# Kernel tuning notes

Measured on AMD Instinct MI355X. Metric: run time of the kernel, lower is better.

Reference implementation:

```python
import jax, jax.numpy as jnp
import numpy as np


def setup_inputs() -> dict:
    key = jax.random.key(0)
    ks = jax.random.split(key, 10)
    B, L, H, E, D = 2, 2048, 16, 64, 64
    d_model = 512
    inp = {
        "queries": jax.random.normal(ks[0], (B, L, H, E), jnp.float32),
        "keys": jax.random.normal(ks[1], (B, L, H, E), jnp.float32),
        "values": jax.random.normal(ks[2], (B, L, H, D), jnp.float32),
        "raw_series": jax.random.normal(ks[3], (B, L, d_model), jnp.float32),
        # learned fusion MLP: Linear(d_model, d_model//2) -> ReLU -> Linear(d_model//2, 1)
        "w1": jax.random.normal(ks[4], (d_model, d_model // 2), jnp.float32) / np.sqrt(d_model),
        "b1": jnp.zeros((d_model // 2,), jnp.float32),
        "w2": jax.random.normal(ks[5], (d_model // 2, 1), jnp.float32) / np.sqrt(d_model // 2),
        "b2": jnp.zeros((1,), jnp.float32),
        # per-head trend scaling, init ones
        "alpha_trend": jnp.ones((H,), jnp.float32),
    }
    return inp


MOMENTUM_ALPHA = 1.0
MOMENTUM_K = 1


def reference(queries, keys, values, raw_series, w1, b1, w2, b2, alpha_trend):
    B, L, H, E = queries.shape
    scale = 1.0 / jnp.sqrt(jnp.asarray(E, queries.dtype))

    # ---- soft momentum bias ----
    # learned fusion: MLP over features -> scalar per position, [B, L]
    h = jax.nn.relu(raw_series @ w1 + b1)
    fused = (h @ w2 + b2)[..., 0]                       # [B, L]
    k = max(1, min(MOMENTUM_K, L - 1))
    momentum = fused[:, k:] - fused[:, :-k]              # [B, L-k]
    momentum = jnp.pad(momentum, ((0, 0), (k, 0)))       # left-pad zeros -> [B, L]
    diff = jnp.abs(momentum[:, :, None] - momentum[:, None, :])  # [B, L, L]
    soft_bias = -MOMENTUM_ALPHA * diff                   # [B, L, L]

    # ---- attention ----
    scores = jnp.einsum('blhe,bshe->bhls', queries, keys)  # [B, H, L, L]
    scores = scores + soft_bias[:, None, :, :] * alpha_trend[None, :, None, None]
    causal = jnp.triu(jnp.ones((L, L), bool), k=1)       # True above diagonal
    scores = jnp.where(causal[None, None], -jnp.inf, scores)
    A = jax.nn.softmax(scale * scores, axis=-1)          # [B, H, L, L]
    V = jnp.einsum('bhls,bshd->blhd', A, values)         # [B, L, H, D]
    return V
```

## Files before the change

kernel.cpp:

```cpp
#include <hip/hip_runtime.h>
#include <math.h>

#define B_ 2
#define L_ 2048
#define H_ 16
#define E_ 64
#define D_ 64
#define DM_ 512
#define DH_ 256

typedef __bf16 bf16_t;
typedef bf16_t bf16x8_t __attribute__((ext_vector_type(8)));
typedef float f32x4_t __attribute__((ext_vector_type(4)));

__device__ __forceinline__ unsigned bpack(float hi, float lo) {
    unsigned uh = __float_as_uint(hi) + 0x8000u;
    unsigned ul = __float_as_uint(lo) + 0x8000u;
    return __builtin_amdgcn_perm(uh, ul, 0x07060302u);
}

__device__ __forceinline__ bf16_t to_bf16(float f) {
    union { float f; unsigned u; } x; x.f = f;
    unsigned r = (x.u + 0x7fffu + ((x.u >> 16) & 1u)) >> 16;
    union { unsigned short s; bf16_t b; } y; y.s = (unsigned short)r;
    return y.b;
}

__global__ __launch_bounds__(256) void transpose_w1_kernel(
        const float* __restrict__ w1, bf16_t* __restrict__ w1t) {
    const int n = blockIdx.x;
    const int t = threadIdx.x;
    #pragma unroll
    for (int u = 0; u < 2; ++u) {
        int k = t + u * 256;
        float v = w1[(size_t)k * DH_ + n];
        w1t[(size_t)n * DM_ + k] = to_bf16(v);
    }
}

__global__ __launch_bounds__(256) void mlp_kernel(
        const float* __restrict__ raw, const bf16_t* __restrict__ w1t,
        const float* __restrict__ b1, const float* __restrict__ w2,
        const float* __restrict__ b2, float* __restrict__ fused) {
    __shared__ bf16_t Rs[16][520];
    __shared__ float part[4][16];
    const int t = threadIdx.x;
    const int m0 = blockIdx.x * 16;
    #pragma unroll
    for (int u = 0; u < 8; ++u) {
        int idx = t + u * 256;
        int row = idx >> 7;
        int k = (idx & 127) << 2;
        f32x4_t v = *(const f32x4_t*)&raw[(size_t)(m0 + row) * DM_ + k];
        uint2 p;
        p.x = bpack(v[1], v[0]);
        p.y = bpack(v[3], v[2]);
        *(uint2*)&Rs[row][k] = p;
    }
    __syncthreads();
    const int wave = t >> 6;
    const int lane = t & 63;
    const int lrow = lane & 15;
    const int lgrp = lane >> 4;
    const int n0w = wave * 64;

    f32x4_t acc[4];
    #pragma unroll
    for (int nt = 0; nt < 4; ++nt) acc[nt] = (f32x4_t){0.f, 0.f, 0.f, 0.f};

    const bf16_t* wbase = w1t + (size_t)(n0w + lrow) * DM_ + lgrp * 8;
    #pragma unroll
    for (int s = 0; s < 16; ++s) {
        bf16x8_t a = *(const bf16x8_t*)&Rs[lrow][s * 32 + lgrp * 8];
        #pragma unroll
        for (int nt = 0; nt < 4; ++nt) {
            bf16x8_t b = *(const bf16x8_t*)(wbase + nt * 16 * DM_ + s * 32);
            acc[nt] = __builtin_amdgcn_mfma_f32_16x16x32_bf16(a, b, acc[nt], 0, 0, 0);
        }
    }
    float rowpart[4] = {0.f, 0.f, 0.f, 0.f};
    #pragma unroll
    for (int nt = 0; nt < 4; ++nt) {
        int n = n0w + nt * 16 + lrow;
        float b1v = b1[n];
        float w2v = w2[n];
        #pragma unroll
        for (int r = 0; r < 4; ++r) {
            float h = acc[nt][r] + b1v;
            h = h > 0.f ? h : 0.f;
            rowpart[r] += h * w2v;
        }
    }
    #pragma unroll
    for (int r = 0; r < 4; ++r) {
        float v = rowpart[r];
        v += __shfl_xor(v, 1);
        v += __shfl_xor(v, 2);
        v += __shfl_xor(v, 4);
        v += __shfl_xor(v, 8);
        if (lrow == 0) part[wave][lgrp * 4 + r] = v;
    }
    __syncthreads();
    if (t < 16)
        fused[m0 + t] = part[0][t] + part[1][t] + part[2][t] + part[3][t] + b2[0];
}

__global__ __launch_bounds__(256) void momentum_kernel(
        const float* __restrict__ fused, float* __restrict__ mom) {
    int i = blockIdx.x * 256 + threadIdx.x;
    if (i < B_ * L_) {
        int l = i & (L_ - 1);
        mom[i] = (l == 0) ? 0.f : fused[i] - fused[i - 1];
    }
}

struct TileRegs { f32x4_t k[4]; float v[16]; float m; };

__global__ __launch_bounds__(256) void attn_kernel(
        const float* __restrict__ Q, const float* __restrict__ K,
        const float* __restrict__ V, const float* __restrict__ mom,
        const float* __restrict__ alpha_trend, float* __restrict__ out) {
    __shared__ bf16_t Ks[64][72];
    __shared__ bf16_t Vt[64][72];
    __shared__ unsigned short Ps[4][16][68];
    __shared__ float moms[64];

    const int bid  = blockIdx.x;
    const int bh   = bid & 31;
    const int qt   = 31 - (bid >> 5);
    const int h    = bh & 15;
    const int b    = bh >> 4;
    const int q0   = qt << 6;
    const int tid  = threadIdx.x;
    const int wave = tid >> 6;
    const int lane = tid & 63;
    const int lrow = lane & 15;
    const int lgrp = lane >> 4;

    const float c1     = 0.18033688f;
    const float ascale2 = alpha_trend[h] * c1;
    const size_t bl    = (size_t)b * L_;
    const int qw0      = q0 + wave * 16;

    const float* Kb   = K + ((bl)*H_ + h) * E_;
    const float* Vb   = V + ((bl)*H_ + h) * D_;
    const float* momp = mom + bl;

    const int krow = tid >> 4;
    const int ke0  = (tid & 15) << 2;
    const int vd   = tid & 63;
    const int vsb  = tid >> 6;

    bf16x8_t a_lo, a_hi;
    {
        const float* qp = Q + ((bl + qw0 + lrow) * H_ + h) * E_ + lgrp * 8;
        f32x4_t v0 = *(const f32x4_t*)(qp);
        f32x4_t v1 = *(const f32x4_t*)(qp + 4);
        f32x4_t v2 = *(const f32x4_t*)(qp + 32);
        f32x4_t v3 = *(const f32x4_t*)(qp + 36);
        #pragma unroll
        for (int k = 0; k < 4; ++k) {
            a_lo[k]     = to_bf16(v0[k] * c1);
            a_lo[4 + k] = to_bf16(v1[k] * c1);
            a_hi[k]     = to_bf16(v2[k] * c1);
            a_hi[4 + k] = to_bf16(v3[k] * c1);
        }
    }
    float mq[4];
    #pragma unroll
    for (int r = 0; r < 4; ++r) mq[r] = momp[qw0 + lgrp * 4 + r];

    f32x4_t Oacc[4];
    #pragma unroll
    for (int c = 0; c < 4; ++c) Oacc[c] = (f32x4_t){0.f, 0.f, 0.f, 0.f};
    float rowsum[4] = {0.f, 0.f, 0.f, 0.f};

    TileRegs tr;
    {
        #pragma unroll
        for (int u = 0; u < 4; ++u)
            tr.k[u] = *(const f32x4_t*)&Kb[(krow + u * 16) * (H_ * E_) + ke0];
        #pragma unroll
        for (int j = 0; j < 16; ++j)
            tr.v[j] = Vb[(vsb * 16 + j) * (H_ * D_) + vd];
        tr.m = (tid < 64) ? momp[tid] : 0.f;
    }

    for (int st = 0; st <= qt; ++st) {
        __syncthreads();
        #pragma unroll
        for (int u = 0; u < 4; ++u) {
            uint2 p;
            p.x = bpack(tr.k[u][1], tr.k[u][0]);
            p.y = bpack(tr.k[u][3], tr.k[u][2]);
            *(uint2*)&Ks[krow + u * 16][ke0] = p;
        }
        #pragma unroll
        for (int u = 0; u < 4; ++u) {
            uint2 p;
            p.x = bpack(tr.v[u * 4 + 1], tr.v[u * 4 + 0]);
            p.y = bpack(tr.v[u * 4 + 3], tr.v[u * 4 + 2]);
            *(uint2*)&Vt[vd][vsb * 16 + u * 4] = p;
        }
        if (tid < 64) moms[tid] = tr.m;
        __syncthreads();

        if (st < qt) {
            const int s0n = (st + 1) << 6;
            #pragma unroll
            for (int u = 0; u < 4; ++u)
                tr.k[u] = *(const f32x4_t*)&Kb[(s0n + krow + u * 16) * (H_ * E_) + ke0];
            #pragma unroll
            for (int j = 0; j < 16; ++j)
                tr.v[j] = Vb[(s0n + vsb * 16 + j) * (H_ * D_) + vd];
            tr.m = (tid < 64) ? momp[s0n + tid] : 0.f;
        }

        f32x4_t Sacc[4];
        #pragma unroll
        for (int c = 0; c < 4; ++c) Sacc[c] = (f32x4_t){0.f, 0.f, 0.f, 0.f};
        #pragma unroll
        for (int c = 0; c < 4; ++c) {
            bf16x8_t b_lo = *(const bf16x8_t*)&Ks[c * 16 + lrow][lgrp * 8];
            bf16x8_t b_hi = *(const bf16x8_t*)&Ks[c * 16 + lrow][32 + lgrp * 8];
            Sacc[c] = __builtin_amdgcn_mfma_f32_16x16x32_bf16(a_lo, b_lo, Sacc[c], 0, 0, 0);
            Sacc[c] = __builtin_amdgcn_mfma_f32_16x16x32_bf16(a_hi, b_hi, Sacc[c], 0, 0, 0);
        }

        float rowe[4][4];
        #pragma unroll
        for (int c = 0; c < 4; ++c) {
            float ms = moms[c * 16 + lrow];
            #pragma unroll
            for (int r = 0; r < 4; ++r) {
                float arg = Sacc[c][r] - ascale2 * fabsf(mq[r] - ms);
                rowe[c][r] = __builtin_amdgcn_exp2f(arg);
            }
        }
        if (st == qt) {
            const int s0 = st << 6;
            #pragma unroll
            for (int c = 0; c < 4; ++c) {
                int sg = s0 + c * 16 + lrow;
                #pragma unroll
                for (int r = 0; r < 4; ++r)
                    if (sg > qw0 + lgrp * 4 + r) rowe[c][r] = 0.f;
            }
        }
        unsigned short* Psw = &Ps[wave][0][0];
        #pragma unroll
        for (int c = 0; c < 4; ++c) {
            #pragma unroll
            for (int r = 0; r < 4; ++r) {
                unsigned u = (__float_as_uint(rowe[c][r]) + 0x8000u) & 0xffff0000u;
                Psw[(lgrp * 4 + r) * 68 + c * 16 + lrow] = (unsigned short)(u >> 16);
                rowsum[r] += __uint_as_float(u);
            }
        }

        #pragma unroll
        for (int hh = 0; hh < 2; ++hh) {
            union { uint2 u2[2]; bf16x8_t v; } ab;
            ab.u2[0] = *(const uint2*)&Psw[lrow * 68 + hh * 32 + lgrp * 8];
            ab.u2[1] = *(const uint2*)&Psw[lrow * 68 + hh * 32 + lgrp * 8 + 4];
            #pragma unroll
            for (int c2 = 0; c2 < 4; ++c2) {
                bf16x8_t bv = *(const bf16x8_t*)&Vt[c2 * 16 + lrow][hh * 32 + lgrp * 8];
                Oacc[c2] = __builtin_amdgcn_mfma_f32_16x16x32_bf16(ab.v, bv, Oacc[c2], 0, 0, 0);
            }
        }
    }

    #pragma unroll
    for (int r = 0; r < 4; ++r) {
        float rs = rowsum[r];
        rs += __shfl_xor(rs, 1);
        rs += __shfl_xor(rs, 2);
        rs += __shfl_xor(rs, 4);
        rs += __shfl_xor(rs, 8);
        float inv = 1.f / rs;
        size_t orow = ((bl + qw0 + lgrp * 4 + r) * H_ + h) * D_;
        #pragma unroll
        for (int c = 0; c < 4; ++c)
            out[orow + c * 16 + lrow] = Oacc[c][r] * inv;
    }
}

extern "C" void kernel_launch(void* const* d_in, const int* in_sizes, int n_in,
                              void* d_out, int out_size, void* d_ws, size_t ws_size,
                              hipStream_t stream) {
    const float* Q     = (const float*)d_in[0];
    const float* K     = (const float*)d_in[1];
    const float* V     = (const float*)d_in[2];
    const float* raw   = (const float*)d_in[3];
    const float* w1    = (const float*)d_in[4];
    const float* b1    = (const float*)d_in[5];
    const float* w2    = (const float*)d_in[6];
    const float* b2    = (const float*)d_in[7];
    const float* alpha = (const float*)d_in[8];
    float* out = (float*)d_out;

    float* fused = (float*)d_ws;
    float* mom   = fused + B_ * L_;
    bf16_t* w1t  = (bf16_t*)(mom + B_ * L_);

    transpose_w1_kernel<<<DH_, 256, 0, stream>>>(w1, w1t);
    mlp_kernel<<<B_ * L_ / 16, 256, 0, stream>>>(raw, w1t, b1, w2, b2, fused);
    momentum_kernel<<<(B_ * L_ + 255) / 256, 256, 0, stream>>>(fused, mom);
    attn_kernel<<<B_ * H_ * (L_ / 64), 256, 0, stream>>>(Q, K, V, mom, alpha, out);
}
```

Baseline: 162.8 us.

## Double-buffer attention K/V tiles, fold momentum into attention, split MLP K across waves

```diff
diff --git a/kernel.cpp b/kernel.cpp
--- a/kernel.cpp
+++ b/kernel.cpp
@@ -38,17 +38,18 @@
     }
 }
 
-__global__ __launch_bounds__(256) void mlp_kernel(
+__global__ __launch_bounds__(512) void mlp_kernel(
         const float* __restrict__ raw, const bf16_t* __restrict__ w1t,
         const float* __restrict__ b1, const float* __restrict__ w2,
         const float* __restrict__ b2, float* __restrict__ fused) {
     __shared__ bf16_t Rs[16][520];
+    __shared__ float pk[4][4][16][17];
     __shared__ float part[4][16];
     const int t = threadIdx.x;
     const int m0 = blockIdx.x * 16;
     #pragma unroll
-    for (int u = 0; u < 8; ++u) {
-        int idx = t + u * 256;
+    for (int u = 0; u < 4; ++u) {
+        int idx = t + u * 512;
         int row = idx >> 7;
         int k = (idx & 127) << 2;
         f32x4_t v = *(const f32x4_t*)&raw[(size_t)(m0 + row) * DM_ + k];
@@ -62,68 +63,72 @@
     const int lane = t & 63;
     const int lrow = lane & 15;
     const int lgrp = lane >> 4;
-    const int n0w = wave * 64;
+    const int nq   = wave & 3;
+    const int kh   = wave >> 2;
+    const int n0w  = nq * 64;
+    const int k0   = kh * 256;
 
     f32x4_t acc[4];
     #pragma unroll
     for (int nt = 0; nt < 4; ++nt) acc[nt] = (f32x4_t){0.f, 0.f, 0.f, 0.f};
 
-    const bf16_t* wbase = w1t + (size_t)(n0w + lrow) * DM_ + lgrp * 8;
-    #pragma unroll
-    for (int s = 0; s < 16; ++s) {
-        bf16x8_t a = *(const bf16x8_t*)&Rs[lrow][s * 32 + lgrp * 8];
+    const bf16_t* wbase = w1t + (size_t)(n0w + lrow) * DM_ + k0 + lgrp * 8;
+    #pragma unroll
+    for (int s = 0; s < 8; ++s) {
+        bf16x8_t a = *(const bf16x8_t*)&Rs[lrow][k0 + s * 32 + lgrp * 8];
         #pragma unroll
         for (int nt = 0; nt < 4; ++nt) {
             bf16x8_t b = *(const bf16x8_t*)(wbase + nt * 16 * DM_ + s * 32);
             acc[nt] = __builtin_amdgcn_mfma_f32_16x16x32_bf16(a, b, acc[nt], 0, 0, 0);
         }
     }
-    float rowpart[4] = {0.f, 0.f, 0.f, 0.f};
-    #pragma unroll
-    for (int nt = 0; nt < 4; ++nt) {
-        int n = n0w + nt * 16 + lrow;
-        float b1v = b1[n];
-        float w2v = w2[n];
+    if (kh == 1) {
+        #pragma unroll
+        for (int nt = 0; nt < 4; ++nt)
+            #pragma unroll
+            for (int r = 0; r < 4; ++r)
+                pk[nq][nt][lgrp * 4 + r][lrow] = acc[nt][r];
+    }
+    __syncthreads();
+    if (kh == 0) {
+        float rowpart[4] = {0.f, 0.f, 0.f, 0.f};
+        #pragma unroll
+        for (int nt = 0; nt < 4; ++nt) {
+            int n = n0w + nt * 16 + lrow;
+            float b1v = b1[n];
+            float w2v = w2[n];
+            #pragma unroll
+            for (int r = 0; r < 4; ++r) {
+                float h = acc[nt][r] + pk[nq][nt][lgrp * 4 + r][lrow] + b1v;
+                h = h > 0.f ? h : 0.f;
+                rowpart[r] += h * w2v;
+            }
+        }
         #pragma unroll
         for (int r = 0; r < 4; ++r) {
-            float h = acc[nt][r] + b1v;
-            h = h > 0.f ? h : 0.f;
-            rowpart[r] += h * w2v;
-        }
-    }
-    #pragma unroll
-    for (int r = 0; r < 4; ++r) {
-        float v = rowpart[r];
-        v += __shfl_xor(v, 1);
-        v += __shfl_xor(v, 2);
-        v += __shfl_xor(v, 4);
-        v += __shfl_xor(v, 8);
-        if (lrow == 0) part[wave][lgrp * 4 + r] = v;
+            float v = rowpart[r];
+            v += __shfl_xor(v, 1);
+            v += __shfl_xor(v, 2);
+            v += __shfl_xor(v, 4);
+            v += __shfl_xor(v, 8);
+            if (lrow == 0) part[nq][lgrp * 4 + r] = v;
+        }
     }
     __syncthreads();
     if (t < 16)
         fused[m0 + t] = part[0][t] + part[1][t] + part[2][t] + part[3][t] + b2[0];
 }
 
-__global__ __launch_bounds__(256) void momentum_kernel(
-        const float* __restrict__ fused, float* __restrict__ mom) {
-    int i = blockIdx.x * 256 + threadIdx.x;
-    if (i < B_ * L_) {
-        int l = i & (L_ - 1);
-        mom[i] = (l == 0) ? 0.f : fused[i] - fused[i - 1];
-    }
-}
-
 struct TileRegs { f32x4_t k[4]; float v[16]; float m; };
 
 __global__ __launch_bounds__(256) void attn_kernel(
         const float* __restrict__ Q, const float* __restrict__ K,
-        const float* __restrict__ V, const float* __restrict__ mom,
+        const float* __restrict__ V, const float* __restrict__ fused,
         const float* __restrict__ alpha_trend, float* __restrict__ out) {
-    __shared__ bf16_t Ks[64][72];
-    __shared__ bf16_t Vt[64][72];
+    __shared__ bf16_t Ks[2][64][72];
+    __shared__ bf16_t Vt[2][64][76];
     __shared__ unsigned short Ps[4][16][68];
-    __shared__ float moms[64];
+    __shared__ float moms[2][64];
 
     const int bid  = blockIdx.x;
     const int bh   = bid & 31;
@@ -137,14 +142,14 @@
     const int lrow = lane & 15;
     const int lgrp = lane >> 4;
 
-    const float c1     = 0.18033688f;
+    const float c1      = 0.18033688f;
     const float ascale2 = alpha_trend[h] * c1;
-    const size_t bl    = (size_t)b * L_;
-    const int qw0      = q0 + wave * 16;
-
-    const float* Kb   = K + ((bl)*H_ + h) * E_;
-    const float* Vb   = V + ((bl)*H_ + h) * D_;
-    const float* momp = mom + bl;
+    const size_t bl     = (size_t)b * L_;
+    const int qw0       = q0 + wave * 16;
+
+    const float* Kb = K + (bl * H_ + h) * E_;
+    const float* Vb = V + (bl * H_ + h) * D_;
+    const float* fp = fused + bl;
 
     const int krow = tid >> 4;
     const int ke0  = (tid & 15) << 2;
@@ -168,7 +173,10 @@
     }
     float mq[4];
     #pragma unroll
-    for (int r = 0; r < 4; ++r) mq[r] = momp[qw0 + lgrp * 4 + r];
+    for (int r = 0; r < 4; ++r) {
+        int l = qw0 + lgrp * 4 + r;
+        mq[r] = (l == 0) ? 0.f : fp[l] - fp[l - 1];
+    }
 
     f32x4_t Oacc[4];
     #pragma unroll
@@ -176,53 +184,55 @@
     float rowsum[4] = {0.f, 0.f, 0.f, 0.f};
 
     TileRegs tr;
-    {
-        #pragma unroll
-        for (int u = 0; u < 4; ++u)
-            tr.k[u] = *(const f32x4_t*)&Kb[(krow + u * 16) * (H_ * E_) + ke0];
-        #pragma unroll
-        for (int j = 0; j < 16; ++j)
-            tr.v[j] = Vb[(vsb * 16 + j) * (H_ * D_) + vd];
-        tr.m = (tid < 64) ? momp[tid] : 0.f;
-    }
+    #define LOAD_TILE(st_) do {                                                   \
+        const int s0_ = (st_) << 6;                                               \
+        _Pragma("unroll")                                                         \
+        for (int u = 0; u < 4; ++u)                                               \
+            tr.k[u] = *(const f32x4_t*)&Kb[(s0_ + krow + u * 16) * (H_ * E_) + ke0]; \
+        _Pragma("unroll")                                                         \
+        for (int j = 0; j < 16; ++j)                                              \
+            tr.v[j] = Vb[(s0_ + vsb * 16 + j) * (H_ * D_) + vd];                  \
+        if (tid < 64) {                                                           \
+            int l_ = s0_ + tid;                                                   \
+            tr.m = (l_ == 0) ? 0.f : fp[l_] - fp[l_ - 1];                         \
+        }                                                                         \
+    } while (0)
+
+    #define STAGE_TILE(pb_) do {                                                  \
+        _Pragma("unroll")                                                         \
+        for (int u = 0; u < 4; ++u) {                                             \
+            uint2 p;                                                              \
+            p.x = bpack(tr.k[u][1], tr.k[u][0]);                                  \
+            p.y = bpack(tr.k[u][3], tr.k[u][2]);                                  \
+            *(uint2*)&Ks[pb_][krow + u * 16][ke0] = p;                            \
+        }                                                                         \
+        _Pragma("unroll")                                                         \
+        for (int u = 0; u < 4; ++u) {                                             \
+            uint2 p;                                                              \
+            p.x = bpack(tr.v[u * 4 + 1], tr.v[u * 4 + 0]);                        \
+            p.y = bpack(tr.v[u * 4 + 3], tr.v[u * 4 + 2]);                        \
+            *(uint2*)&Vt[pb_][vd][vsb * 16 + u * 4] = p;                          \
+        }                                                                         \
+        if (tid < 64) moms[pb_][tid] = tr.m;                                      \
+    } while (0)
+
+    LOAD_TILE(0);
+    STAGE_TILE(0);
+    if (qt >= 1) LOAD_TILE(1);
+    __syncthreads();
 
     for (int st = 0; st <= qt; ++st) {
-        __syncthreads();
-        #pragma unroll
-        for (int u = 0; u < 4; ++u) {
-            uint2 p;
-            p.x = bpack(tr.k[u][1], tr.k[u][0]);
-            p.y = bpack(tr.k[u][3], tr.k[u][2]);
-            *(uint2*)&Ks[krow + u * 16][ke0] = p;
-        }
-        #pragma unroll
-        for (int u = 0; u < 4; ++u) {
-            uint2 p;
-            p.x = bpack(tr.v[u * 4 + 1], tr.v[u * 4 + 0]);
-            p.y = bpack(tr.v[u * 4 + 3], tr.v[u * 4 + 2]);
-            *(uint2*)&Vt[vd][vsb * 16 + u * 4] = p;
-        }
-        if (tid < 64) moms[tid] = tr.m;
-        __syncthreads();
-
-        if (st < qt) {
-            const int s0n = (st + 1) << 6;
-            #pragma unroll
-            for (int u = 0; u < 4; ++u)
-                tr.k[u] = *(const f32x4_t*)&Kb[(s0n + krow + u * 16) * (H_ * E_) + ke0];
-            #pragma unroll
-            for (int j = 0; j < 16; ++j)
-                tr.v[j] = Vb[(s0n + vsb * 16 + j) * (H_ * D_) + vd];
-            tr.m = (tid < 64) ? momp[s0n + tid] : 0.f;
-        }
+        const int cb = st & 1;
+        if (st < qt) STAGE_TILE((st + 1) & 1);
+        if (st + 2 <= qt) LOAD_TILE(st + 2);
 
         f32x4_t Sacc[4];
         #pragma unroll
         for (int c = 0; c < 4; ++c) Sacc[c] = (f32x4_t){0.f, 0.f, 0.f, 0.f};
         #pragma unroll
         for (int c = 0; c < 4; ++c) {
-            bf16x8_t b_lo = *(const bf16x8_t*)&Ks[c * 16 + lrow][lgrp * 8];
-            bf16x8_t b_hi = *(const bf16x8_t*)&Ks[c * 16 + lrow][32 + lgrp * 8];
+            bf16x8_t b_lo = *(const bf16x8_t*)&Ks[cb][c * 16 + lrow][lgrp * 8];
+            bf16x8_t b_hi = *(const bf16x8_t*)&Ks[cb][c * 16 + lrow][32 + lgrp * 8];
             Sacc[c] = __builtin_amdgcn_mfma_f32_16x16x32_bf16(a_lo, b_lo, Sacc[c], 0, 0, 0);
             Sacc[c] = __builtin_amdgcn_mfma_f32_16x16x32_bf16(a_hi, b_hi, Sacc[c], 0, 0, 0);
         }
@@ -230,7 +240,7 @@
         float rowe[4][4];
         #pragma unroll
         for (int c = 0; c < 4; ++c) {
-            float ms = moms[c * 16 + lrow];
+            float ms = moms[cb][c * 16 + lrow];
             #pragma unroll
             for (int r = 0; r < 4; ++r) {
                 float arg = Sacc[c][r] - ascale2 * fabsf(mq[r] - ms);
@@ -265,10 +275,13 @@
             ab.u2[1] = *(const uint2*)&Psw[lrow * 68 + hh * 32 + lgrp * 8 + 4];
             #pragma unroll
             for (int c2 = 0; c2 < 4; ++c2) {
-                bf16x8_t bv = *(const bf16x8_t*)&Vt[c2 * 16 + lrow][hh * 32 + lgrp * 8];
-                Oacc[c2] = __builtin_amdgcn_mfma_f32_16x16x32_bf16(ab.v, bv, Oacc[c2], 0, 0, 0);
-            }
-        }
+                union { uint2 u2[2]; bf16x8_t v; } bb;
+                bb.u2[0] = *(const uint2*)&Vt[cb][c2 * 16 + lrow][hh * 32 + lgrp * 8];
+                bb.u2[1] = *(const uint2*)&Vt[cb][c2 * 16 + lrow][hh * 32 + lgrp * 8 + 4];
+                Oacc[c2] = __builtin_amdgcn_mfma_f32_16x16x32_bf16(ab.v, bb.v, Oacc[c2], 0, 0, 0);
+            }
+        }
+        __syncthreads();
     }
 
     #pragma unroll
@@ -284,6 +297,8 @@
         for (int c = 0; c < 4; ++c)
             out[orow + c * 16 + lrow] = Oacc[c][r] * inv;
     }
+    #undef LOAD_TILE
+    #undef STAGE_TILE
 }
 
 extern "C" void kernel_launch(void* const* d_in, const int* in_sizes, int n_in,
@@ -301,11 +316,9 @@
     float* out = (float*)d_out;
 
     float* fused = (float*)d_ws;
-    float* mom   = fused + B_ * L_;
-    bf16_t* w1t  = (bf16_t*)(mom + B_ * L_);
+    bf16_t* w1t  = (bf16_t*)(fused + B_ * L_);
 
     transpose_w1_kernel<<<DH_, 256, 0, stream>>>(w1, w1t);
-    mlp_kernel<<<B_ * L_ / 16, 256, 0, stream>>>(raw, w1t, b1, w2, b2, fused);
-    momentum_kernel<<<(B_ * L_ + 255) / 256, 256, 0, stream>>>(fused, mom);
-    attn_kernel<<<B_ * H_ * (L_ / 64), 256, 0, stream>>>(Q, K, V, mom, alpha, out);
-}
+    mlp_kernel<<<B_ * L_ / 16, 512, 0, stream>>>(raw, w1t, b1, w2, b2, fused);
+    attn_kernel<<<B_ * H_ * (L_ / 64), 256, 0, stream>>>(Q, K, V, fused, alpha, out);
+}
```

After: 170.9 us. +4.9%, slower.
